# Kernel optimization log

Measured on AMD Instinct MI355X. Metric: run time of the kernel, lower is better.

Reference implementation:

```python
import jax, jax.numpy as jnp
import numpy as np

NUM_FEATURES = 8
HIDDEN_DIM = 256
NUM_STABILIZERS = 2048
B, S = 128, 2048


def setup_inputs() -> dict:
    key = jax.random.key(0)
    ks = jax.random.split(key, 8)
    x = jax.random.normal(ks[0], (B, S, NUM_FEATURES), dtype=jnp.float32)
    final_mask = jax.random.randint(ks[1], (B, S), 0, 3, dtype=jnp.int64)
    # stacked per-feature Linear(1, hidden): W[f, h] = weight of proj f, b[f, h] = bias
    xav = float(np.sqrt(6.0 / (1 + HIDDEN_DIM)))  # xavier_uniform for Linear(1, H)
    W = jax.random.uniform(ks[2], (NUM_FEATURES, HIDDEN_DIM), minval=-xav, maxval=xav, dtype=jnp.float32)
    b = jnp.zeros((NUM_FEATURES, HIDDEN_DIM), dtype=jnp.float32)
    index_embed = 0.02 * jax.random.normal(ks[3], (NUM_STABILIZERS, HIDDEN_DIM), dtype=jnp.float32)
    final_on = jax.random.normal(ks[4], (HIDDEN_DIM,), dtype=jnp.float32)
    final_off = jax.random.normal(ks[5], (HIDDEN_DIM,), dtype=jnp.float32)
    gamma = jnp.ones((HIDDEN_DIM,), dtype=jnp.float32)
    beta = jnp.zeros((HIDDEN_DIM,), dtype=jnp.float32)
    return {"x": x, "final_mask": final_mask, "W": W, "b": b,
            "index_embed": index_embed, "final_on": final_on,
            "final_off": final_off, "gamma": gamma, "beta": beta}


def reference(x, final_mask, W, b, index_embed, final_on, final_off, gamma, beta):
    Bx, Sx, _ = x.shape
    # sum of per-feature Linear(1,H): single GEMM + summed bias
    h = jnp.einsum('bsf,fh->bsh', x, W) + b.sum(axis=0)  # [B,S,H]
    h = h + index_embed[:Sx][None, :, :]
    h = h + (final_mask == 1)[..., None] * final_on
    h = h + (final_mask == 2)[..., None] * final_off
    # LayerNorm over last dim, eps=1e-5 (torch default)
    mu = h.mean(axis=-1, keepdims=True)
    var = h.var(axis=-1, keepdims=True)
    h = (h - mu) * jax.lax.rsqrt(var + 1e-5)
    return h * gamma + beta
```

## Files before the change

kernel.cpp:

```cpp
#include <hip/hip_runtime.h>

#define HID 256
#define NFEAT 8
#define SLEN 2048

typedef float v4f __attribute__((ext_vector_type(4)));

__device__ __forceinline__ float wave_sum(float v) {
#pragma unroll
    for (int o = 32; o > 0; o >>= 1) v += __shfl_xor(v, o, 64);
    return v;
}

__global__ __launch_bounds__(64) void k1_build(
    const float* __restrict__ bias, const float* __restrict__ ie,
    const float* __restrict__ W,    const float* __restrict__ fon,
    const float* __restrict__ foff,
    float* __restrict__ base2, float* __restrict__ tab, float* __restrict__ cst)
{
    const int lane = threadIdx.x;
    const int h0 = lane << 2;

    float wc[NFEAT][4];
#pragma unroll
    for (int f = 0; f < NFEAT; ++f) {
        const float4 w4 = *reinterpret_cast<const float4*>(W + f * HID + h0);
        wc[f][0] = w4.x; wc[f][1] = w4.y; wc[f][2] = w4.z; wc[f][3] = w4.w;
    }
    const float4 on4 = *reinterpret_cast<const float4*>(fon  + h0);
    const float4 of4 = *reinterpret_cast<const float4*>(foff + h0);
    const float on[4]  = {on4.x, on4.y, on4.z, on4.w};
    const float off[4] = {of4.x, of4.y, of4.z, of4.w};

    if (blockIdx.x < SLEN) {
        const int s = blockIdx.x;
        const float4 e4 = *reinterpret_cast<const float4*>(ie + (size_t)s * HID + h0);
        float b0[4] = {e4.x, e4.y, e4.z, e4.w};
#pragma unroll
        for (int f = 0; f < NFEAT; ++f) {
            const float4 b4 = *reinterpret_cast<const float4*>(bias + f * HID + h0);
            b0[0] += b4.x; b0[1] += b4.y; b0[2] += b4.z; b0[3] += b4.w;
        }
        float r[12];
        r[0] = b0[0] + b0[1] + b0[2] + b0[3];
        r[1] = b0[0]*b0[0] + b0[1]*b0[1] + b0[2]*b0[2] + b0[3]*b0[3];
        r[2] = b0[0]*on[0] + b0[1]*on[1] + b0[2]*on[2] + b0[3]*on[3];
        r[3] = b0[0]*off[0]+ b0[1]*off[1]+ b0[2]*off[2]+ b0[3]*off[3];
#pragma unroll
        for (int f = 0; f < NFEAT; ++f)
            r[4+f] = b0[0]*wc[f][0] + b0[1]*wc[f][1] + b0[2]*wc[f][2] + b0[3]*wc[f][3];
#pragma unroll
        for (int i = 0; i < 12; ++i) r[i] = wave_sum(r[i]);

        float4 b04 = make_float4(b0[0], b0[1], b0[2], b0[3]);
        *reinterpret_cast<float4*>(base2 + (size_t)s * HID + h0) = b04;
        if (lane == 0) {
#pragma unroll
            for (int i = 0; i < 12; ++i) tab[s * 16 + i] = r[i];
        }
    } else {
        float r[92];
#pragma unroll
        for (int f = 0; f < NFEAT; ++f)
#pragma unroll
            for (int g = 0; g < NFEAT; ++g)
                r[f*8+g] = wc[f][0]*wc[g][0] + wc[f][1]*wc[g][1]
                         + wc[f][2]*wc[g][2] + wc[f][3]*wc[g][3];
#pragma unroll
        for (int f = 0; f < NFEAT; ++f)
            r[64+f] = wc[f][0] + wc[f][1] + wc[f][2] + wc[f][3];
#pragma unroll
        for (int f = 0; f < NFEAT; ++f)
            r[72+f] = on[0]*wc[f][0] + on[1]*wc[f][1] + on[2]*wc[f][2] + on[3]*wc[f][3];
#pragma unroll
        for (int f = 0; f < NFEAT; ++f)
            r[80+f] = off[0]*wc[f][0] + off[1]*wc[f][1] + off[2]*wc[f][2] + off[3]*wc[f][3];
        r[88] = on[0] + on[1] + on[2] + on[3];
        r[89] = off[0]+ off[1]+ off[2]+ off[3];
        r[90] = on[0]*on[0] + on[1]*on[1] + on[2]*on[2] + on[3]*on[3];
        r[91] = off[0]*off[0]+ off[1]*off[1]+ off[2]*off[2]+ off[3]*off[3];
#pragma unroll
        for (int i = 0; i < 92; ++i) r[i] = wave_sum(r[i]);
        if (lane == 0) {
#pragma unroll
            for (int i = 0; i < 92; ++i) cst[i] = r[i];
        }
    }
}

__global__ __launch_bounds__(256, 4) void k2_stats(
    const float* __restrict__ x, const int* __restrict__ mask,
    const float* __restrict__ tab, const float* __restrict__ cst,
    float2* __restrict__ musig, int Bdim)
{
    const int tid   = blockIdx.x * blockDim.x + threadIdx.x;
    const int lane  = tid & 63;
    const int gwave = tid >> 6;
    const int b     = gwave >> 5;
    const int s     = ((gwave & 31) << 6) + lane;
    if (b >= Bdim) return;
    const int t = b * SLEN + s;

    const float4 x0 = *reinterpret_cast<const float4*>(x + (size_t)t * NFEAT);
    const float4 x1 = *reinterpret_cast<const float4*>(x + (size_t)t * NFEAT + 4);
    const float xs[NFEAT] = {x0.x, x0.y, x0.z, x0.w, x1.x, x1.y, x1.z, x1.w};
    const int m = mask[t];
    const float fm1 = (m == 1) ? 1.0f : 0.0f;
    const float fm2 = (m == 2) ? 1.0f : 0.0f;

    const float4* tab4 = reinterpret_cast<const float4*>(tab + (size_t)s * 16);
    const float4 t0 = tab4[0];
    const float4 q0 = tab4[1];
    const float4 q1 = tab4[2];
    float qf[NFEAT] = {q0.x, q0.y, q0.z, q0.w, q1.x, q1.y, q1.z, q1.w};

    const float4* c4 = reinterpret_cast<const float4*>(cst);
    const float4 sw0 = c4[16], sw1 = c4[17];
    const float4 so0 = c4[18], so1 = c4[19];
    const float4 sf0 = c4[20], sf1 = c4[21];
    const float4 sc  = c4[22];
    const float sw[NFEAT]   = {sw0.x, sw0.y, sw0.z, sw0.w, sw1.x, sw1.y, sw1.z, sw1.w};
    const float sonw[NFEAT] = {so0.x, so0.y, so0.z, so0.w, so1.x, so1.y, so1.z, so1.w};
    const float sofw[NFEAT] = {sf0.x, sf0.y, sf0.z, sf0.w, sf1.x, sf1.y, sf1.z, sf1.w};

#pragma unroll
    for (int f = 0; f < NFEAT; ++f)
        qf[f] += fm1 * sonw[f] + fm2 * sofw[f];

    float s1 = t0.x + fm1 * sc.x + fm2 * sc.y;
#pragma unroll
    for (int f = 0; f < NFEAT; ++f) s1 = fmaf(xs[f], sw[f], s1);

    float s2 = t0.y + fm1 * (2.0f * t0.z + sc.z) + fm2 * (2.0f * t0.w + sc.w);
#pragma unroll
    for (int f = 0; f < NFEAT; ++f) {
        const float4 wa = c4[f * 2];
        const float4 wb = c4[f * 2 + 1];
        float tf = 2.0f * qf[f];
        tf = fmaf(wa.x, xs[0], tf); tf = fmaf(wa.y, xs[1], tf);
        tf = fmaf(wa.z, xs[2], tf); tf = fmaf(wa.w, xs[3], tf);
        tf = fmaf(wb.x, xs[4], tf); tf = fmaf(wb.y, xs[5], tf);
        tf = fmaf(wb.z, xs[6], tf); tf = fmaf(wb.w, xs[7], tf);
        s2 = fmaf(xs[f], tf, s2);
    }

    const float mu   = s1 * (1.0f / HID);
    const float var  = s2 * (1.0f / HID) - mu * mu;
    const float rstd = rsqrtf(var + 1e-5f);
    musig[t] = make_float2(mu, rstd);
}

__global__ __launch_bounds__(256, 4) void k3_apply(
    const float* __restrict__ x, const int* __restrict__ mask,
    const float* __restrict__ W, const float* __restrict__ base2,
    const float* __restrict__ fon, const float* __restrict__ foff,
    const float* __restrict__ gamma, const float* __restrict__ beta,
    const float2* __restrict__ musig, float* __restrict__ out, int ntokens)
{
    const int lane = threadIdx.x & 63;
    const int wavesPerBlock = blockDim.x >> 6;
    const int gwave = blockIdx.x * wavesPerBlock + (threadIdx.x >> 6);
    const int nwaves = gridDim.x * wavesPerBlock;
    const int h0 = lane << 2;

    float wc[NFEAT][4];
#pragma unroll
    for (int f = 0; f < NFEAT; ++f) {
        const float4 w4 = *reinterpret_cast<const float4*>(W + f * HID + h0);
        wc[f][0] = w4.x; wc[f][1] = w4.y; wc[f][2] = w4.z; wc[f][3] = w4.w;
    }
    const float4 g4  = *reinterpret_cast<const float4*>(gamma + h0);
    const float4 be4 = *reinterpret_cast<const float4*>(beta  + h0);
    const float4 on4 = *reinterpret_cast<const float4*>(fon   + h0);
    const float4 of4 = *reinterpret_cast<const float4*>(foff  + h0);

    auto process = [&](int t) {
        const int s = t & (SLEN - 1);
        const float2 ms = musig[t];
        float4 acc = *reinterpret_cast<const float4*>(base2 + (size_t)s * HID + h0);
        const float4 x0 = *reinterpret_cast<const float4*>(x + (size_t)t * NFEAT);
        const float4 x1 = *reinterpret_cast<const float4*>(x + (size_t)t * NFEAT + 4);
        const int m = mask[t];
        if (m == 1) {
            acc.x += on4.x; acc.y += on4.y; acc.z += on4.z; acc.w += on4.w;
        } else if (m == 2) {
            acc.x += of4.x; acc.y += of4.y; acc.z += of4.z; acc.w += of4.w;
        }
        const float xs[NFEAT] = {x0.x, x0.y, x0.z, x0.w, x1.x, x1.y, x1.z, x1.w};
#pragma unroll
        for (int f = 0; f < NFEAT; ++f) {
            acc.x = fmaf(xs[f], wc[f][0], acc.x);
            acc.y = fmaf(xs[f], wc[f][1], acc.y);
            acc.z = fmaf(xs[f], wc[f][2], acc.z);
            acc.w = fmaf(xs[f], wc[f][3], acc.w);
        }
        v4f o;
        o.x = (acc.x - ms.x) * ms.y * g4.x + be4.x;
        o.y = (acc.y - ms.x) * ms.y * g4.y + be4.y;
        o.z = (acc.z - ms.x) * ms.y * g4.z + be4.z;
        o.w = (acc.w - ms.x) * ms.y * g4.w + be4.w;
        __builtin_nontemporal_store(o, reinterpret_cast<v4f*>(out + (size_t)t * HID + h0));
    };

    int t = gwave;
    for (; t + nwaves < ntokens; t += 2 * nwaves) {
        process(t);
        process(t + nwaves);
    }
    if (t < ntokens) process(t);
}

extern "C" void kernel_launch(void* const* d_in, const int* in_sizes, int n_in,
                              void* d_out, int out_size, void* d_ws, size_t ws_size,
                              hipStream_t stream) {
    const float* x     = (const float*)d_in[0];
    const int*   mask  = (const int*)  d_in[1];
    const float* W     = (const float*)d_in[2];
    const float* bias  = (const float*)d_in[3];
    const float* ie    = (const float*)d_in[4];
    const float* fon   = (const float*)d_in[5];
    const float* foff  = (const float*)d_in[6];
    const float* gamma = (const float*)d_in[7];
    const float* beta  = (const float*)d_in[8];
    float* out = (float*)d_out;

    const int ntokens = in_sizes[0] / NFEAT;
    const int Bdim    = ntokens / SLEN;

    char* ws = (char*)d_ws;
    float*  base2 = (float*)(ws);
    float*  tab   = (float*)(ws + (1u << 21));
    float*  cst   = (float*)(ws + (1u << 21) + (1u << 18));
    float2* musig = (float2*)(ws + (1u << 21) + (1u << 18) + (1u << 16));

    k1_build<<<SLEN + 1, 64, 0, stream>>>(bias, ie, W, fon, foff, base2, tab, cst);

    {
        const int blocks = (Bdim * 32 * 64) / 256;
        k2_stats<<<blocks, 256, 0, stream>>>(x, mask, tab, cst, musig, Bdim);
    }

    k3_apply<<<2048, 256, 0, stream>>>(
        x, mask, W, base2, fon, foff, gamma, beta, musig, out, ntokens);
}
```

Before: 341.1 us.

## Fold gamma into precomputed tables and load weights per token in apply kernel

The build kernel now premultiplies the base table, W, final_on and final_off by gamma. This lets the apply kernel compute out = acc*rstd + (beta - mu*rstd*gamma) with fewer multiplies and no per-thread register copy of W, and its occupancy hint is raised to 6. The build kernel packs 4 sequence positions per 256-thread block and computes the constant dot products with one thread each instead of wave reductions. The output store changes from nontemporal to a normal store, which may pollute cache on a large write-bound output.

```diff
diff --git a/kernel.cpp b/kernel.cpp
--- a/kernel.cpp
+++ b/kernel.cpp
@@ -4,36 +4,38 @@
 #define NFEAT 8
 #define SLEN 2048
 
-typedef float v4f __attribute__((ext_vector_type(4)));
-
 __device__ __forceinline__ float wave_sum(float v) {
 #pragma unroll
     for (int o = 32; o > 0; o >>= 1) v += __shfl_xor(v, o, 64);
     return v;
 }
 
-__global__ __launch_bounds__(64) void k1_build(
+__global__ __launch_bounds__(256) void k1_build(
     const float* __restrict__ bias, const float* __restrict__ ie,
     const float* __restrict__ W,    const float* __restrict__ fon,
-    const float* __restrict__ foff,
-    float* __restrict__ base2, float* __restrict__ tab, float* __restrict__ cst)
+    const float* __restrict__ foff, const float* __restrict__ gamma,
+    float* __restrict__ base2g, float* __restrict__ tab, float* __restrict__ cst,
+    float* __restrict__ wg, float* __restrict__ ong, float* __restrict__ offg)
 {
-    const int lane = threadIdx.x;
-    const int h0 = lane << 2;
-
-    float wc[NFEAT][4];
-#pragma unroll
-    for (int f = 0; f < NFEAT; ++f) {
-        const float4 w4 = *reinterpret_cast<const float4*>(W + f * HID + h0);
-        wc[f][0] = w4.x; wc[f][1] = w4.y; wc[f][2] = w4.z; wc[f][3] = w4.w;
-    }
-    const float4 on4 = *reinterpret_cast<const float4*>(fon  + h0);
-    const float4 of4 = *reinterpret_cast<const float4*>(foff + h0);
-    const float on[4]  = {on4.x, on4.y, on4.z, on4.w};
-    const float off[4] = {of4.x, of4.y, of4.z, of4.w};
-
-    if (blockIdx.x < SLEN) {
-        const int s = blockIdx.x;
+    const int tid = threadIdx.x;
+
+    if (blockIdx.x < SLEN / 4) {
+        const int lane = tid & 63;
+        const int s = blockIdx.x * 4 + (tid >> 6);
+        const int h0 = lane << 2;
+
+        float wc[NFEAT][4];
+#pragma unroll
+        for (int f = 0; f < NFEAT; ++f) {
+            const float4 w4 = *reinterpret_cast<const float4*>(W + f * HID + h0);
+            wc[f][0] = w4.x; wc[f][1] = w4.y; wc[f][2] = w4.z; wc[f][3] = w4.w;
+        }
+        const float4 on4 = *reinterpret_cast<const float4*>(fon  + h0);
+        const float4 of4 = *reinterpret_cast<const float4*>(foff + h0);
+        const float4 g4  = *reinterpret_cast<const float4*>(gamma + h0);
+        const float on[4]  = {on4.x, on4.y, on4.z, on4.w};
+        const float off[4] = {of4.x, of4.y, of4.z, of4.w};
+
         const float4 e4 = *reinterpret_cast<const float4*>(ie + (size_t)s * HID + h0);
         float b0[4] = {e4.x, e4.y, e4.z, e4.w};
 #pragma unroll
@@ -41,6 +43,7 @@
             const float4 b4 = *reinterpret_cast<const float4*>(bias + f * HID + h0);
             b0[0] += b4.x; b0[1] += b4.y; b0[2] += b4.z; b0[3] += b4.w;
         }
+
         float r[12];
         r[0] = b0[0] + b0[1] + b0[2] + b0[3];
         r[1] = b0[0]*b0[0] + b0[1]*b0[1] + b0[2]*b0[2] + b0[3]*b0[3];
@@ -52,38 +55,74 @@
 #pragma unroll
         for (int i = 0; i < 12; ++i) r[i] = wave_sum(r[i]);
 
-        float4 b04 = make_float4(b0[0], b0[1], b0[2], b0[3]);
-        *reinterpret_cast<float4*>(base2 + (size_t)s * HID + h0) = b04;
+        float4 bg = make_float4(b0[0]*g4.x, b0[1]*g4.y, b0[2]*g4.z, b0[3]*g4.w);
+        *reinterpret_cast<float4*>(base2g + (size_t)s * HID + h0) = bg;
         if (lane == 0) {
 #pragma unroll
             for (int i = 0; i < 12; ++i) tab[s * 16 + i] = r[i];
         }
     } else {
-        float r[92];
-#pragma unroll
-        for (int f = 0; f < NFEAT; ++f)
-#pragma unroll
-            for (int g = 0; g < NFEAT; ++g)
-                r[f*8+g] = wc[f][0]*wc[g][0] + wc[f][1]*wc[g][1]
-                         + wc[f][2]*wc[g][2] + wc[f][3]*wc[g][3];
-#pragma unroll
-        for (int f = 0; f < NFEAT; ++f)
-            r[64+f] = wc[f][0] + wc[f][1] + wc[f][2] + wc[f][3];
-#pragma unroll
-        for (int f = 0; f < NFEAT; ++f)
-            r[72+f] = on[0]*wc[f][0] + on[1]*wc[f][1] + on[2]*wc[f][2] + on[3]*wc[f][3];
-#pragma unroll
-        for (int f = 0; f < NFEAT; ++f)
-            r[80+f] = off[0]*wc[f][0] + off[1]*wc[f][1] + off[2]*wc[f][2] + off[3]*wc[f][3];
-        r[88] = on[0] + on[1] + on[2] + on[3];
-        r[89] = off[0]+ off[1]+ off[2]+ off[3];
-        r[90] = on[0]*on[0] + on[1]*on[1] + on[2]*on[2] + on[3]*on[3];
-        r[91] = off[0]*off[0]+ off[1]*off[1]+ off[2]*off[2]+ off[3]*off[3];
-#pragma unroll
-        for (int i = 0; i < 92; ++i) r[i] = wave_sum(r[i]);
-        if (lane == 0) {
-#pragma unroll
-            for (int i = 0; i < 92; ++i) cst[i] = r[i];
+        if (tid < 92) {
+            float acc = 0.0f;
+            if (tid < 64) {
+                const int f = tid >> 3, g = tid & 7;
+                for (int h = 0; h < HID; h += 4) {
+                    const float4 a = *reinterpret_cast<const float4*>(W + f * HID + h);
+                    const float4 b = *reinterpret_cast<const float4*>(W + g * HID + h);
+                    acc = fmaf(a.x, b.x, acc); acc = fmaf(a.y, b.y, acc);
+                    acc = fmaf(a.z, b.z, acc); acc = fmaf(a.w, b.w, acc);
+                }
+            } else if (tid < 72) {
+                const int f = tid - 64;
+                for (int h = 0; h < HID; h += 4) {
+                    const float4 a = *reinterpret_cast<const float4*>(W + f * HID + h);
+                    acc += a.x + a.y + a.z + a.w;
+                }
+            } else if (tid < 80) {
+                const int f = tid - 72;
+                for (int h = 0; h < HID; h += 4) {
+                    const float4 a = *reinterpret_cast<const float4*>(W + f * HID + h);
+                    const float4 b = *reinterpret_cast<const float4*>(fon + h);
+                    acc = fmaf(a.x, b.x, acc); acc = fmaf(a.y, b.y, acc);
+                    acc = fmaf(a.z, b.z, acc); acc = fmaf(a.w, b.w, acc);
+                }
+            } else if (tid < 88) {
+                const int f = tid - 80;
+                for (int h = 0; h < HID; h += 4) {
+                    const float4 a = *reinterpret_cast<const float4*>(W + f * HID + h);
+                    const float4 b = *reinterpret_cast<const float4*>(foff + h);
+                    acc = fmaf(a.x, b.x, acc); acc = fmaf(a.y, b.y, acc);
+                    acc = fmaf(a.z, b.z, acc); acc = fmaf(a.w, b.w, acc);
+                }
+            } else {
+                const float* p = (tid == 88 || tid == 90) ? fon : foff;
+                const bool sq = (tid >= 90);
+                for (int h = 0; h < HID; h += 4) {
+                    const float4 a = *reinterpret_cast<const float4*>(p + h);
+                    if (sq) {
+                        acc = fmaf(a.x, a.x, acc); acc = fmaf(a.y, a.y, acc);
+                        acc = fmaf(a.z, a.z, acc); acc = fmaf(a.w, a.w, acc);
+                    } else {
+                        acc += a.x + a.y + a.z + a.w;
+                    }
+                }
+            }
+            cst[tid] = acc;
+        }
+        for (int idx = tid; idx < NFEAT * (HID / 4); idx += 256) {
+            const int f = idx >> 6, h4 = (idx & 63) << 2;
+            const float4 a = *reinterpret_cast<const float4*>(W + f * HID + h4);
+            const float4 g = *reinterpret_cast<const float4*>(gamma + h4);
+            float4 r = make_float4(a.x*g.x, a.y*g.y, a.z*g.z, a.w*g.w);
+            *reinterpret_cast<float4*>(wg + f * HID + h4) = r;
+        }
+        if (tid < HID / 4) {
+            const int h4 = tid << 2;
+            const float4 g = *reinterpret_cast<const float4*>(gamma + h4);
+            const float4 a = *reinterpret_cast<const float4*>(fon + h4);
+            const float4 b = *reinterpret_cast<const float4*>(foff + h4);
+            *reinterpret_cast<float4*>(ong + h4)  = make_float4(a.x*g.x, a.y*g.y, a.z*g.z, a.w*g.w);
+            *reinterpret_cast<float4*>(offg + h4) = make_float4(b.x*g.x, b.y*g.y, b.z*g.z, b.w*g.w);
         }
     }
 }
@@ -150,10 +189,10 @@
     musig[t] = make_float2(mu, rstd);
 }
 
-__global__ __launch_bounds__(256, 4) void k3_apply(
+__global__ __launch_bounds__(256, 6) void k3_apply(
     const float* __restrict__ x, const int* __restrict__ mask,
-    const float* __restrict__ W, const float* __restrict__ base2,
-    const float* __restrict__ fon, const float* __restrict__ foff,
+    const float* __restrict__ base2g, const float* __restrict__ wg,
+    const float* __restrict__ ong, const float* __restrict__ offg,
     const float* __restrict__ gamma, const float* __restrict__ beta,
     const float2* __restrict__ musig, float* __restrict__ out, int ntokens)
 {
@@ -163,21 +202,15 @@
     const int nwaves = gridDim.x * wavesPerBlock;
     const int h0 = lane << 2;
 
-    float wc[NFEAT][4];
-#pragma unroll
-    for (int f = 0; f < NFEAT; ++f) {
-        const float4 w4 = *reinterpret_cast<const float4*>(W + f * HID + h0);
-        wc[f][0] = w4.x; wc[f][1] = w4.y; wc[f][2] = w4.z; wc[f][3] = w4.w;
-    }
     const float4 g4  = *reinterpret_cast<const float4*>(gamma + h0);
     const float4 be4 = *reinterpret_cast<const float4*>(beta  + h0);
-    const float4 on4 = *reinterpret_cast<const float4*>(fon   + h0);
-    const float4 of4 = *reinterpret_cast<const float4*>(foff  + h0);
+    const float4 on4 = *reinterpret_cast<const float4*>(ong   + h0);
+    const float4 of4 = *reinterpret_cast<const float4*>(offg  + h0);
 
     auto process = [&](int t) {
         const int s = t & (SLEN - 1);
         const float2 ms = musig[t];
-        float4 acc = *reinterpret_cast<const float4*>(base2 + (size_t)s * HID + h0);
+        float4 acc = *reinterpret_cast<const float4*>(base2g + (size_t)s * HID + h0);
         const float4 x0 = *reinterpret_cast<const float4*>(x + (size_t)t * NFEAT);
         const float4 x1 = *reinterpret_cast<const float4*>(x + (size_t)t * NFEAT + 4);
         const int m = mask[t];
@@ -189,17 +222,19 @@
         const float xs[NFEAT] = {x0.x, x0.y, x0.z, x0.w, x1.x, x1.y, x1.z, x1.w};
 #pragma unroll
         for (int f = 0; f < NFEAT; ++f) {
-            acc.x = fmaf(xs[f], wc[f][0], acc.x);
-            acc.y = fmaf(xs[f], wc[f][1], acc.y);
-            acc.z = fmaf(xs[f], wc[f][2], acc.z);
-            acc.w = fmaf(xs[f], wc[f][3], acc.w);
-        }
-        v4f o;
-        o.x = (acc.x - ms.x) * ms.y * g4.x + be4.x;
-        o.y = (acc.y - ms.x) * ms.y * g4.y + be4.y;
-        o.z = (acc.z - ms.x) * ms.y * g4.z + be4.z;
-        o.w = (acc.w - ms.x) * ms.y * g4.w + be4.w;
-        __builtin_nontemporal_store(o, reinterpret_cast<v4f*>(out + (size_t)t * HID + h0));
+            const float4 w4 = *reinterpret_cast<const float4*>(wg + f * HID + h0);
+            acc.x = fmaf(xs[f], w4.x, acc.x);
+            acc.y = fmaf(xs[f], w4.y, acc.y);
+            acc.z = fmaf(xs[f], w4.z, acc.z);
+            acc.w = fmaf(xs[f], w4.w, acc.w);
+        }
+        const float c = ms.x * ms.y;
+        float4 o4;
+        o4.x = fmaf(acc.x, ms.y, fmaf(-c, g4.x, be4.x));
+        o4.y = fmaf(acc.y, ms.y, fmaf(-c, g4.y, be4.y));
+        o4.z = fmaf(acc.z, ms.y, fmaf(-c, g4.z, be4.z));
+        o4.w = fmaf(acc.w, ms.y, fmaf(-c, g4.w, be4.w));
+        *reinterpret_cast<float4*>(out + (size_t)t * HID + h0) = o4;
     };
 
     int t = gwave;
@@ -228,18 +263,19 @@
     const int Bdim    = ntokens / SLEN;
 
     char* ws = (char*)d_ws;
-    float*  base2 = (float*)(ws);
-    float*  tab   = (float*)(ws + (1u << 21));
-    float*  cst   = (float*)(ws + (1u << 21) + (1u << 18));
-    float2* musig = (float2*)(ws + (1u << 21) + (1u << 18) + (1u << 16));
-
-    k1_build<<<SLEN + 1, 64, 0, stream>>>(bias, ie, W, fon, foff, base2, tab, cst);
-
-    {
-        const int blocks = (Bdim * 32 * 64) / 256;
-        k2_stats<<<blocks, 256, 0, stream>>>(x, mask, tab, cst, musig, Bdim);
-    }
+    float*  base2g = (float*)(ws);
+    float*  tab    = (float*)(ws + (1u << 21));
+    float*  wg     = (float*)(ws + (1u << 21) + (1u << 17));
+    float*  ong    = (float*)(ws + (1u << 21) + (1u << 17) + (1u<<13));
+    float*  offg   = (float*)(ws + (1u << 21) + (1u << 17) + (1u<<13) + (1u<<10));
+    float*  cst    = (float*)(ws + (1u << 21) + (1u << 17) + (1u<<14));
+    float2* musig  = (float2*)(ws + (1u << 21) + (1u << 18));
+
+    k1_build<<<SLEN / 4 + 1, 256, 0, stream>>>(
+        bias, ie, W, fon, foff, gamma, base2g, tab, cst, wg, ong, offg);
+
+    k2_stats<<<Bdim * 8, 256, 0, stream>>>(x, mask, tab, cst, musig, Bdim);
 
     k3_apply<<<2048, 256, 0, stream>>>(
-        x, mask, W, base2, fon, foff, gamma, beta, musig, out, ntokens);
-}
+        x, mask, base2g, wg, ong, offg, gamma, beta, musig, out, ntokens);
+}
```

New measurement: 347.4 us. About the same (+1.9%).
